# Kernel optimization log

Hardware: AMD Instinct MI355X
Metric: run time of the kernel (lower is better)

The kernel has to match this reference:

```python
import jax, jax.numpy as jnp
import numpy as np

DT_SCALER = 1.0 / 24.0
ODE_STEPS = 4  # fixed-step RK4 stand-in for adaptive odeint(rtol=atol=1e-3)
B, T, D, H = 1024, 100, 32, 256
ODE_MID = 50  # hidden width of the ODE func MLP (hard-coded 50 in source)


def setup_inputs() -> dict:
    key = jax.random.key(0)
    ks = jax.random.split(key, 20)
    n = lambda k, s: jax.random.normal(k, s, dtype=jnp.float32)
    std = 0.1  # module inits weights N(0, 0.1), biases 0
    return {
        "dt": jax.random.uniform(ks[0], (B, T, 2), dtype=jnp.float32),
        "x": n(ks[1], (B, T, D)),
        # RNNCell params
        "W_ih": n(ks[2], (H, D)) * std,
        "b_ih": jnp.zeros((H,), jnp.float32),
        "W_hh": n(ks[3], (H, H)) * std,
        "b_hh": jnp.zeros((H,), jnp.float32),
        # ODE func: Linear(H,50) -> tanh -> Linear(50,H)
        "ode_w1": n(ks[4], (ODE_MID, H)) * std,
        "ode_b1": jnp.zeros((ODE_MID,), jnp.float32),
        "ode_w2": n(ks[5], (H, ODE_MID)) * std,
        "ode_b2": jnp.zeros((H,), jnp.float32),
        # mu head: l1 (H -> H//2), distribution_mu (H//2 -> 1)
        "l1_w": n(ks[6], (H // 2, H)) * std,
        "l1_b": jnp.zeros((H // 2,), jnp.float32),
        "mu_w": n(ks[7], (1, H // 2)) * std,
        "mu_b": jnp.zeros((1,), jnp.float32),
        # sigma head: Linear(H,H) -> tanh -> Linear(H,1) -> softplus
        "sig_w1": n(ks[8], (H, H)) * std,
        "sig_b1": jnp.zeros((H,), jnp.float32),
        "sig_w2": n(ks[9], (1, H)) * std,
        "sig_b2": jnp.zeros((1,), jnp.float32),
    }


def reference(dt, x, W_ih, b_ih, W_hh, b_hh, ode_w1, ode_b1, ode_w2, ode_b2,
              l1_w, l1_b, mu_w, mu_b, sig_w1, sig_b1, sig_w2, sig_b2):
    Bsz = x.shape[0]
    xs = jnp.swapaxes(x, 0, 1)                               # [T,B,D]
    dts = jnp.swapaxes(dt[:, :, 1] - dt[:, :, 0], 0, 1)[..., None]  # [T,B,1]
    h0 = jnp.zeros((Bsz, W_hh.shape[0]), x.dtype)
    hs = 1.0 / ODE_STEPS

    def ode_f(y, scale):
        # net(y) * (dt * DT_SCALER); RHS is time-independent
        return (jnp.tanh(y @ ode_w1.T + ode_b1) @ ode_w2.T + ode_b2) * scale

    def step(h, inp):
        x_i, dt_i = inp                                      # [B,D], [B,1]
        # h_t = h_t + RNNCell(x_i, h_t)
        h = h + jnp.tanh(x_i @ W_ih.T + b_ih + h @ W_hh.T + b_hh)
        scale = dt_i * DT_SCALER
        # integrate dh/dt = ode_f(h) from t=0 to t=1 (fixed-step RK4)
        def rk4(y, _):
            k1 = ode_f(y, scale)
            k2 = ode_f(y + 0.5 * hs * k1, scale)
            k3 = ode_f(y + 0.5 * hs * k2, scale)
            k4 = ode_f(y + hs * k3, scale)
            return y + (hs / 6.0) * (k1 + 2.0 * k2 + 2.0 * k3 + k4), None
        h, _ = jax.lax.scan(rk4, h, None, length=ODE_STEPS)
        # heads (eval mode: dropout is identity)
        mu = jax.nn.relu(h @ l1_w.T + l1_b) @ mu_w.T + mu_b              # [B,1]
        sig = jax.nn.softplus(jnp.tanh(h @ sig_w1.T + sig_b1) @ sig_w2.T + sig_b2)
        return h, (mu, sig)

    _, (mu_seq, sig_seq) = jax.lax.scan(step, h0, (xs, dts))
    mu_out = jnp.swapaxes(mu_seq, 0, 1)    # [B,T,1]
    sig_out = jnp.swapaxes(sig_seq, 0, 1)  # [B,T,1]
    return (mu_out, sig_out)
```

## Files before the change

kernel.cpp:

```cpp
#include <hip/hip_runtime.h>
#include <math.h>


#define NT 512

#define WS_WCAT 0
#define WS_L1P  73728
#define WS_SW1  106496
#define WS_TOT  172032

#define F4_PR1P 0
#define F4_PR1Q 1088
#define F4_PR2P 2176
#define F4_PR2Q 3216
#define F4_PRR  2176
#define F4_PH1  0
#define F4_PH2  2176
#define F4_YCP  4256
#define F4_YCQ  4384
#define F4_MIDP 4512
#define F4_MIDQ 4544
#define F4_HS   4576
#define F4_XS   4832
#define F4_L1O  4864
#define F4_SG   4992
#define F4_END  5248
#define SM_BC   (F4_END * 4)
#define SM_OB1  (SM_BC + 256)
#define SM_OB2  (SM_OB1 + 64)
#define SM_L1B  (SM_OB2 + 256)
#define SM_SB1  (SM_L1B + 128)
#define SM_MUW  (SM_SB1 + 256)
#define SM_SW2  (SM_MUW + 128)
#define SM_SCL  (SM_SW2 + 256)
#define SM_TOTF (SM_SCL + 8)
#define SMEM_BYTES (SM_TOTF * 4)

__device__ __forceinline__ float fma4(float acc, float4 y, float4 w) {
  acc = fmaf(y.x, w.x, acc); acc = fmaf(y.y, w.y, acc);
  acc = fmaf(y.z, w.z, acc); acc = fmaf(y.w, w.w, acc);
  return acc;
}
__device__ __forceinline__ float4 add4(float4 a, float4 b) {
  return make_float4(a.x + b.x, a.y + b.y, a.z + b.z, a.w + b.w);
}
__device__ __forceinline__ float4 axpy4(float a, float4 xv, float4 yv) {
  return make_float4(fmaf(a, xv.x, yv.x), fmaf(a, xv.y, yv.y),
                     fmaf(a, xv.z, yv.z), fmaf(a, xv.w, yv.w));
}
__device__ __forceinline__ float4 muls4(float4 v, float s) {
  return make_float4(v.x * s, v.y * s, v.z * s, v.w * s);
}
__device__ __forceinline__ float tfast(float x) {
  float ax = fabsf(x);
  float e  = __expf(-2.f * ax);
  float t  = (1.f - e) * __builtin_amdgcn_rcpf(1.f + e);
  return copysignf(t, x);
}
__device__ __forceinline__ float4 tfast4(float4 v) {
  return make_float4(tfast(v.x), tfast(v.y), tfast(v.z), tfast(v.w));
}
template <int CTRL>
__device__ __forceinline__ float dpp_add(float v) {
  int s = __builtin_amdgcn_update_dpp(0, __float_as_int(v), CTRL, 0xF, 0xF, true);
  return v + __int_as_float(s);
}
__device__ __forceinline__ float4 red4f4(float4 v) {
  v.x = dpp_add<0xB1>(v.x); v.y = dpp_add<0xB1>(v.y);
  v.z = dpp_add<0xB1>(v.z); v.w = dpp_add<0xB1>(v.w);
  v.x = dpp_add<0x4E>(v.x); v.y = dpp_add<0x4E>(v.y);
  v.z = dpp_add<0x4E>(v.z); v.w = dpp_add<0x4E>(v.w);
  return v;
}

__global__ void prep_w(const float* __restrict__ Wih, const float* __restrict__ Whh,
                       const float* __restrict__ l1w, const float* __restrict__ sw1,
                       float* __restrict__ ws) {
  int i = blockIdx.x * 256 + threadIdx.x;
  if (i < 73728) {
    int g = i >> 10, rem = i & 1023, j = rem >> 2, c = rem & 3;
    int k = 4 * g + c;
    ws[i] = (k < 32) ? Wih[j * 32 + k] : Whh[j * 256 + (k - 32)];
  } else if (i < 106496) {
    int t = i - 73728;
    int g = t >> 9, rem = t & 511, j = rem >> 2, c = rem & 3;
    ws[i] = l1w[j * 256 + 4 * g + c];
  } else if (i < WS_TOT) {
    int t = i - 106496;
    int g = t >> 10, rem = t & 1023, j = rem >> 2, c = rem & 3;
    ws[i] = sw1[j * 256 + 4 * g + c];
  }
}

__global__ __attribute__((amdgpu_flat_work_group_size(NT, NT)))
void odernn_main(const float* __restrict__ dt,
                 const float* __restrict__ x,
                 const float* __restrict__ bih,
                 const float* __restrict__ bhh,
                 const float* __restrict__ ow1,
                 const float* __restrict__ ob1g,
                 const float* __restrict__ ow2,
                 const float* __restrict__ ob2g,
                 const float* __restrict__ l1bg,
                 const float* __restrict__ muwg,
                 const float* __restrict__ mubg,
                 const float* __restrict__ sb1g,
                 const float* __restrict__ sw2g,
                 const float* __restrict__ sb2g,
                 const float* __restrict__ ws,
                 float* __restrict__ out) {
  extern __shared__ __align__(16) float sm[];
  float4* f4 = (float4*)sm;
  const int tid = threadIdx.x;
  const int b0 = blockIdx.x * 4;

  const float4* wcat4 = (const float4*)(ws + WS_WCAT);
  const float4* l1w4  = (const float4*)(ws + WS_L1P);
  const float4* sw14  = (const float4*)(ws + WS_SW1);
  const float4* xg4   = (const float4*)x;

  const int q1 = tid & 15, kc1 = tid >> 4;
  const int cq2 = tid & 63, kc2 = tid >> 6;
  float4 w1r[4][2];
  float4 w2r[4][2];
  {
#pragma unroll
    for (int n = 0; n < 4; ++n) {
      int row = 4 * q1 + n;
#pragma unroll
      for (int g = 0; g < 2; ++g) {
        if (row < 50)
          w1r[n][g] = *(const float4*)&ow1[row * 256 + kc1 * 8 + 4 * g];
        else
          w1r[n][g] = make_float4(0.f, 0.f, 0.f, 0.f);
      }
    }
    float w2tmp[4];
#pragma unroll
    for (int n = 0; n < 4; ++n) {
      int col = 4 * cq2 + n;
#pragma unroll
      for (int g = 0; g < 2; ++g) {
#pragma unroll
        for (int c = 0; c < 4; ++c) {
          int k = kc2 * 8 + 4 * g + c;
          w2tmp[c] = (k < 50) ? ow2[col * 50 + k] : 0.f;
        }
        w2r[n][g] = make_float4(w2tmp[0], w2tmp[1], w2tmp[2], w2tmp[3]);
      }
    }
  }

  if (tid < 256) {
    sm[SM_BC + tid]  = bih[tid] + bhh[tid];
    sm[SM_OB2 + tid] = ob2g[tid];
    sm[SM_SB1 + tid] = sb1g[tid];
    sm[SM_SW2 + tid] = sw2g[tid];
  }
  if (tid < 64)  sm[SM_OB1 + tid] = (tid < 50) ? ob1g[tid] : 0.f;
  if (tid < 128) { sm[SM_L1B + tid] = l1bg[tid]; sm[SM_MUW + tid] = muwg[tid]; }
  if (tid < 256) f4[F4_HS + tid] = make_float4(0.f, 0.f, 0.f, 0.f);
  if (tid < 32) {
    int r = tid >> 3, g = tid & 7;
    f4[F4_XS + tid] = xg4[((size_t)(b0 + r) * 100) * 8 + g];
  } else if (tid < 36) {
    int r = tid - 32;
    const float* dp = dt + ((size_t)(b0 + r) * 100) * 2;
    sm[SM_SCL + r] = (dp[1] - dp[0]) * (1.f / 24.f);
  }
  __syncthreads();

  const float mubv = mubg[0], sb2v = sb2g[0];
  const float4* bc4   = (const float4*)(sm + SM_BC);
  const float4* ob1_4 = (const float4*)(sm + SM_OB1);
  const float4* ob2_4 = (const float4*)(sm + SM_OB2);
  const float4* l1b4  = (const float4*)(sm + SM_L1B);
  const float4* sb14  = (const float4*)(sm + SM_SB1);
  const float4* muw4  = (const float4*)(sm + SM_MUW);
  const float4* sw24  = (const float4*)(sm + SM_SW2);

  const int cqS = tid & 63, rxS = (tid >> 6) & 1;
  float4 hP = make_float4(0, 0, 0, 0), acP = hP, hQ = hP, acQ = hP;
  float scP = 0.f, scQ = 0.f;

  const int wv = tid >> 6, ln = tid & 63;

  auto L1PART = [&](int ycB, int prB) {
    float4 p0 = make_float4(0, 0, 0, 0), p1 = p0;
#pragma unroll
    for (int g = 0; g < 2; ++g) {
      float4 y0 = f4[ycB + kc1 * 2 + g];
      float4 y1 = f4[ycB + 64 + kc1 * 2 + g];
      p0.x = fma4(p0.x, y0, w1r[0][g]); p0.y = fma4(p0.y, y0, w1r[1][g]);
      p0.z = fma4(p0.z, y0, w1r[2][g]); p0.w = fma4(p0.w, y0, w1r[3][g]);
      p1.x = fma4(p1.x, y1, w1r[0][g]); p1.y = fma4(p1.y, y1, w1r[1][g]);
      p1.z = fma4(p1.z, y1, w1r[2][g]); p1.w = fma4(p1.w, y1, w1r[3][g]);
    }
    f4[prB + (kc1 * 2 + 0) * 17 + q1] = p0;
    f4[prB + (kc1 * 2 + 1) * 17 + q1] = p1;
  };
  auto L1RED = [&](int prB, int midB) {
    const int qr = (tid >> 2) & 15, sub = tid & 3, rx = tid >> 6;
    float4 v = make_float4(0, 0, 0, 0);
#pragma unroll
    for (int i = 0; i < 8; ++i)
      v = add4(v, f4[prB + ((sub * 8 + i) * 2 + rx) * 17 + qr]);
    v = red4f4(v);
    if (sub == 0)
      f4[midB + rx * 16 + qr] = tfast4(add4(v, ob1_4[qr]));
  };
  auto L2PART = [&](int midB, int prB) {
    float4 p0 = make_float4(0, 0, 0, 0), p1 = p0;
#pragma unroll
    for (int g = 0; g < 2; ++g) {
      float4 m0 = f4[midB + kc2 * 2 + g];
      float4 m1 = f4[midB + 16 + kc2 * 2 + g];
      p0.x = fma4(p0.x, m0, w2r[0][g]); p0.y = fma4(p0.y, m0, w2r[1][g]);
      p0.z = fma4(p0.z, m0, w2r[2][g]); p0.w = fma4(p0.w, m0, w2r[3][g]);
      p1.x = fma4(p1.x, m1, w2r[0][g]); p1.y = fma4(p1.y, m1, w2r[1][g]);
      p1.z = fma4(p1.z, m1, w2r[2][g]); p1.w = fma4(p1.w, m1, w2r[3][g]);
    }
    f4[prB + (kc2 * 2 + 0) * 65 + cq2] = p0;
    f4[prB + (kc2 * 2 + 1) * 65 + cq2] = p1;
  };
  auto L2RED = [&](float4& h, float4& ac, float sc, int prB, int ycB,
                   int hsRow, int e) {
    float4 v = ob2_4[cqS];
#pragma unroll
    for (int i = 0; i < 8; ++i)
      v = add4(v, f4[prB + (i * 2 + rxS) * 65 + cqS]);
    float4 kv = muls4(v, sc);
    const int s = e & 3;
    float4 ycw;
    if (s == 0) {
      ac = kv;                      ycw = axpy4(0.125f, kv, h);
    } else if (s == 1) {
      ac = axpy4(2.f, kv, ac);      ycw = axpy4(0.125f, kv, h);
    } else if (s == 2) {
      ac = axpy4(2.f, kv, ac);      ycw = axpy4(0.25f, kv, h);
    } else {
      h = axpy4(0.25f / 6.f, add4(ac, kv), h);
      ycw = h;
    }
    f4[ycB + rxS * 64 + cqS] = ycw;
    if (e == 15) f4[F4_HS + hsRow * 64 + cqS] = h;
  };

  for (int t = 0; t < 100; ++t) {
    {
      const int jq = tid & 63, kc = tid >> 6;
      float4 a0 = make_float4(0, 0, 0, 0), a1 = a0, a2 = a0, a3 = a0;
#pragma unroll 3
      for (int gg = 0; gg < 9; ++gg) {
        int g = kc * 9 + gg;
        float4 w0 = wcat4[g * 256 + 4 * jq + 0];
        float4 w1 = wcat4[g * 256 + 4 * jq + 1];
        float4 w2 = wcat4[g * 256 + 4 * jq + 2];
        float4 w3 = wcat4[g * 256 + 4 * jq + 3];
        float4 y0 = (g < 8) ? f4[F4_XS + g]      : f4[F4_HS + (g - 8)];
        float4 y1 = (g < 8) ? f4[F4_XS + 8 + g]  : f4[F4_HS + 64 + (g - 8)];
        float4 y2 = (g < 8) ? f4[F4_XS + 16 + g] : f4[F4_HS + 128 + (g - 8)];
        float4 y3 = (g < 8) ? f4[F4_XS + 24 + g] : f4[F4_HS + 192 + (g - 8)];
        a0.x = fma4(a0.x, y0, w0); a0.y = fma4(a0.y, y0, w1);
        a0.z = fma4(a0.z, y0, w2); a0.w = fma4(a0.w, y0, w3);
        a1.x = fma4(a1.x, y1, w0); a1.y = fma4(a1.y, y1, w1);
        a1.z = fma4(a1.z, y1, w2); a1.w = fma4(a1.w, y1, w3);
        a2.x = fma4(a2.x, y2, w0); a2.y = fma4(a2.y, y2, w1);
        a2.z = fma4(a2.z, y2, w2); a2.w = fma4(a2.w, y2, w3);
        a3.x = fma4(a3.x, y3, w0); a3.y = fma4(a3.y, y3, w1);
        a3.z = fma4(a3.z, y3, w2); a3.w = fma4(a3.w, y3, w3);
      }
      f4[F4_PRR + (kc * 4 + 0) * 65 + jq] = a0;
      f4[F4_PRR + (kc * 4 + 1) * 65 + jq] = a1;
      f4[F4_PRR + (kc * 4 + 2) * 65 + jq] = a2;
      f4[F4_PRR + (kc * 4 + 3) * 65 + jq] = a3;
    }
    __syncthreads();
    if (tid < 256) {
      const int r = tid >> 6, jq = tid & 63;
      float4 v = bc4[jq];
#pragma unroll
      for (int kc = 0; kc < 8; ++kc)
        v = add4(v, f4[F4_PRR + (kc * 4 + r) * 65 + jq]);
      float4 hn = add4(f4[F4_HS + r * 64 + jq], tfast4(v));
      if (r < 2) f4[F4_YCP + r * 64 + jq] = hn;
      else       f4[F4_YCQ + (r - 2) * 64 + jq] = hn;
    }
    __syncthreads();

#pragma unroll 1
    for (int e = 0; e < 16; ++e) {
      L1PART(F4_YCP, F4_PR1P);
      if (tid < 128) {
        if (e == 0) {
          hP = f4[F4_YCP + rxS * 64 + cqS];
          hQ = f4[F4_YCQ + rxS * 64 + cqS];
          acP = make_float4(0, 0, 0, 0); acQ = acP;
          scP = sm[SM_SCL + rxS];
          scQ = sm[SM_SCL + 2 + rxS];
        } else {
          L2RED(hQ, acQ, scQ, F4_PR2Q, F4_YCQ, 2 + rxS, e - 1);
        }
      }
      __syncthreads();
      L1PART(F4_YCQ, F4_PR1Q);
      if (tid < 128) L1RED(F4_PR1P, F4_MIDP);
      __syncthreads();
      L2PART(F4_MIDP, F4_PR2P);
      if (tid < 128) L1RED(F4_PR1Q, F4_MIDQ);
      __syncthreads();
      L2PART(F4_MIDQ, F4_PR2Q);
      if (tid < 128) L2RED(hP, acP, scP, F4_PR2P, F4_YCP, 0 + rxS, e);
      __syncthreads();
    }
    if (tid < 128) {
      L2RED(hQ, acQ, scQ, F4_PR2Q, F4_YCQ, 2 + rxS, 15);
    } else if (t < 99) {
      if (tid < 160) {
        int idx = tid - 128, r = idx >> 3, g = idx & 7;
        f4[F4_XS + idx] = xg4[((size_t)(b0 + r) * 100 + t + 1) * 8 + g];
      } else if (tid < 164) {
        int r = tid - 160;
        const float* dp = dt + ((size_t)(b0 + r) * 100 + t + 1) * 2;
        sm[SM_SCL + r] = (dp[1] - dp[0]) * (1.f / 24.f);
      }
    }
    __syncthreads();

    {
      const int cq = tid & 31, kc = tid >> 5;
      float4 c0 = make_float4(0, 0, 0, 0), c1 = c0, c2 = c0, c3 = c0;
#pragma unroll 2
      for (int g = 0; g < 4; ++g) {
        int kg = kc * 4 + g;
        float4 w0 = l1w4[kg * 128 + 4 * cq + 0];
        float4 w1 = l1w4[kg * 128 + 4 * cq + 1];
        float4 w2 = l1w4[kg * 128 + 4 * cq + 2];
        float4 w3 = l1w4[kg * 128 + 4 * cq + 3];
        float4 y0 = f4[F4_HS + kg],       y1 = f4[F4_HS + 64 + kg];
        float4 y2 = f4[F4_HS + 128 + kg], y3 = f4[F4_HS + 192 + kg];
        c0.x = fma4(c0.x, y0, w0); c0.y = fma4(c0.y, y0, w1);
        c0.z = fma4(c0.z, y0, w2); c0.w = fma4(c0.w, y0, w3);
        c1.x = fma4(c1.x, y1, w0); c1.y = fma4(c1.y, y1, w1);
        c1.z = fma4(c1.z, y1, w2); c1.w = fma4(c1.w, y1, w3);
        c2.x = fma4(c2.x, y2, w0); c2.y = fma4(c2.y, y2, w1);
        c2.z = fma4(c2.z, y2, w2); c2.w = fma4(c2.w, y2, w3);
        c3.x = fma4(c3.x, y3, w0); c3.y = fma4(c3.y, y3, w1);
        c3.z = fma4(c3.z, y3, w2); c3.w = fma4(c3.w, y3, w3);
      }
      f4[F4_PH1 + (kc * 4 + 0) * 33 + cq] = c0;
      f4[F4_PH1 + (kc * 4 + 1) * 33 + cq] = c1;
      f4[F4_PH1 + (kc * 4 + 2) * 33 + cq] = c2;
      f4[F4_PH1 + (kc * 4 + 3) * 33 + cq] = c3;
    }
    {
      const int cq = tid & 63, kc = tid >> 6;
      float4 d0 = make_float4(0, 0, 0, 0), d1 = d0, d2 = d0, d3 = d0;
#pragma unroll 2
      for (int g = 0; g < 8; ++g) {
        int kg = kc * 8 + g;
        float4 w0 = sw14[kg * 256 + 4 * cq + 0];
        float4 w1 = sw14[kg * 256 + 4 * cq + 1];
        float4 w2 = sw14[kg * 256 + 4 * cq + 2];
        float4 w3 = sw14[kg * 256 + 4 * cq + 3];
        float4 y0 = f4[F4_HS + kg],       y1 = f4[F4_HS + 64 + kg];
        float4 y2 = f4[F4_HS + 128 + kg], y3 = f4[F4_HS + 192 + kg];
        d0.x = fma4(d0.x, y0, w0); d0.y = fma4(d0.y, y0, w1);
        d0.z = fma4(d0.z, y0, w2); d0.w = fma4(d0.w, y0, w3);
        d1.x = fma4(d1.x, y1, w0); d1.y = fma4(d1.y, y1, w1);
        d1.z = fma4(d1.z, y1, w2); d1.w = fma4(d1.w, y1, w3);
        d2.x = fma4(d2.x, y2, w0); d2.y = fma4(d2.y, y2, w1);
        d2.z = fma4(d2.z, y2, w2); d2.w = fma4(d2.w, y2, w3);
        d3.x = fma4(d3.x, y3, w0); d3.y = fma4(d3.y, y3, w1);
        d3.z = fma4(d3.z, y3, w2); d3.w = fma4(d3.w, y3, w3);
      }
      f4[F4_PH2 + (kc * 4 + 0) * 65 + cq] = d0;
      f4[F4_PH2 + (kc * 4 + 1) * 65 + cq] = d1;
      f4[F4_PH2 + (kc * 4 + 2) * 65 + cq] = d2;
      f4[F4_PH2 + (kc * 4 + 3) * 65 + cq] = d3;
    }
    __syncthreads();
    if (tid < 128) {
      const int r = tid >> 5, cq = tid & 31;
      float4 v = l1b4[cq];
#pragma unroll
      for (int kc = 0; kc < 16; ++kc)
        v = add4(v, f4[F4_PH1 + (kc * 4 + r) * 33 + cq]);
      f4[F4_L1O + r * 32 + cq] =
          make_float4(fmaxf(v.x, 0.f), fmaxf(v.y, 0.f),
                      fmaxf(v.z, 0.f), fmaxf(v.w, 0.f));
    } else if (tid < 384) {
      const int t2 = tid - 128;
      const int r = t2 >> 6, cq = t2 & 63;
      float4 v = sb14[cq];
#pragma unroll
      for (int kc = 0; kc < 8; ++kc)
        v = add4(v, f4[F4_PH2 + (kc * 4 + r) * 65 + cq]);
      f4[F4_SG + r * 64 + cq] = tfast4(v);
    }
    __syncthreads();
    if (wv < 4) {
      float pm = 0.f;
      if (ln < 32) {
        float4 l = f4[F4_L1O + wv * 32 + ln];
        float4 w = muw4[ln];
        pm = l.x * w.x + l.y * w.y + l.z * w.z + l.w * w.w;
      }
#pragma unroll
      for (int off = 32; off > 0; off >>= 1) pm += __shfl_down(pm, off);
      if (ln == 0) out[(size_t)(b0 + wv) * 100 + t] = pm + mubv;
    } else {
      const int r = wv - 4;
      float4 sv = f4[F4_SG + r * 64 + ln];
      float4 w = sw24[ln];
      float ps = sv.x * w.x + sv.y * w.y + sv.z * w.z + sv.w * w.w;
#pragma unroll
      for (int off = 32; off > 0; off >>= 1) ps += __shfl_down(ps, off);
      if (ln == 0) {
        float z = ps + sb2v;
        float sp = fmaxf(z, 0.f) + log1pf(expf(-fabsf(z)));
        out[(size_t)102400 + (size_t)(b0 + r) * 100 + t] = sp;
      }
    }
    __syncthreads();
  }
}

extern "C" void kernel_launch(void* const* d_in, const int* in_sizes, int n_in,
                              void* d_out, int out_size, void* d_ws, size_t ws_size,
                              hipStream_t stream) {
  const float* dt  = (const float*)d_in[0];
  const float* x   = (const float*)d_in[1];
  const float* Wih = (const float*)d_in[2];
  const float* bih = (const float*)d_in[3];
  const float* Whh = (const float*)d_in[4];
  const float* bhh = (const float*)d_in[5];
  const float* ow1 = (const float*)d_in[6];
  const float* ob1 = (const float*)d_in[7];
  const float* ow2 = (const float*)d_in[8];
  const float* ob2 = (const float*)d_in[9];
  const float* l1w = (const float*)d_in[10];
  const float* l1b = (const float*)d_in[11];
  const float* muw = (const float*)d_in[12];
  const float* mub = (const float*)d_in[13];
  const float* sw1 = (const float*)d_in[14];
  const float* sb1 = (const float*)d_in[15];
  const float* sw2 = (const float*)d_in[16];
  const float* sb2 = (const float*)d_in[17];
  float* ws  = (float*)d_ws;
  float* out = (float*)d_out;

  hipFuncSetAttribute((const void*)odernn_main,
                      hipFuncAttributeMaxDynamicSharedMemorySize, SMEM_BYTES);

  prep_w<<<WS_TOT / 256, 256, 0, stream>>>(Wih, Whh, l1w, sw1, ws);
  odernn_main<<<256, NT, SMEM_BYTES, stream>>>(dt, x, bih, bhh, ow1, ob1, ow2, ob2,
                                               l1b, muw, mub, sb1, sw2, sb2, ws, out);
}
```

Measured before the change: 4.077 ms.

## Split ODE MLP layers across wave pairs with register-resident weights

Halves the block to 256 threads. Even waves now compute the first ODE layer (H→50, tanh) for one batch row while odd waves compute the second layer and the RK4 update for the other row, so the two layers run as a ping-pong pipeline over 33 phases per time step. Both ODE weight matrices are staged once in shared memory and reloaded into registers each step, and the layer-1 partial sums are reduced across lanes with DPP instead of through shared memory. This removes shared-memory partial-sum round trips and some barriers, at the cost of heavy register pressure (52 float4 weights per thread) and half as many threads for the RNN and head matmuls.

After: 3.323 ms. -18.5%, faster.

```diff
diff --git a/kernel.cpp b/kernel.cpp
--- a/kernel.cpp
+++ b/kernel.cpp
@@ -2,54 +2,48 @@
 #include <math.h>
 
 
-#define NT 512
+#define NT 256
 
 #define WS_WCAT 0
 #define WS_L1P  73728
 #define WS_SW1  106496
 #define WS_TOT  172032
 
-#define F4_PR1P 0
-#define F4_PR1Q 1088
-#define F4_PR2P 2176
-#define F4_PR2Q 3216
-#define F4_PRR  2176
-#define F4_PH1  0
-#define F4_PH2  2176
-#define F4_YCP  4256
-#define F4_YCQ  4384
-#define F4_MIDP 4512
-#define F4_MIDQ 4544
-#define F4_HS   4576
-#define F4_XS   4832
-#define F4_L1O  4864
-#define F4_SG   4992
-#define F4_END  5248
-#define SM_BC   (F4_END * 4)
-#define SM_OB1  (SM_BC + 256)
-#define SM_OB2  (SM_OB1 + 64)
-#define SM_L1B  (SM_OB2 + 256)
-#define SM_SB1  (SM_L1B + 128)
-#define SM_MUW  (SM_SB1 + 256)
-#define SM_SW2  (SM_MUW + 128)
-#define SM_SCL  (SM_SW2 + 256)
-#define SM_TOTF (SM_SCL + 8)
-#define SMEM_BYTES (SM_TOTF * 4)
-
-__device__ __forceinline__ float fma4(float acc, float4 y, float4 w) {
-  acc = fmaf(y.x, w.x, acc); acc = fmaf(y.y, w.y, acc);
-  acc = fmaf(y.z, w.z, acc); acc = fmaf(y.w, w.w, acc);
-  return acc;
+#define F4_YC   0
+#define F4_MID  256
+#define F4_PRR  320
+#define F4_PH1  320
+#define F4_PH2  1376
+#define F4_XS   2416
+#define F4_L1O  2448
+#define F4_SG   2576
+#define F4_W1   2832
+#define F4_W2   6160
+#define F4_END  9488
+#define SM_BC   (F4_END*4)
+#define SM_OB2  (SM_BC+256)
+#define SM_L1B  (SM_OB2+256)
+#define SM_SB1  (SM_L1B+128)
+#define SM_MUW  (SM_SB1+256)
+#define SM_SW2  (SM_MUW+128)
+#define SM_SCL  (SM_SW2+256)
+#define SM_TOTF (SM_SCL+4)
+#define SMEM_BYTES (SM_TOTF*4)
+
+__device__ __forceinline__ float fma4(float a, float4 y, float4 w) {
+  a = fmaf(y.x, w.x, a); a = fmaf(y.y, w.y, a);
+  a = fmaf(y.z, w.z, a); a = fmaf(y.w, w.w, a);
+  return a;
 }
 __device__ __forceinline__ float4 add4(float4 a, float4 b) {
-  return make_float4(a.x + b.x, a.y + b.y, a.z + b.z, a.w + b.w);
+  return make_float4(a.x+b.x, a.y+b.y, a.z+b.z, a.w+b.w);
 }
 __device__ __forceinline__ float4 axpy4(float a, float4 xv, float4 yv) {
-  return make_float4(fmaf(a, xv.x, yv.x), fmaf(a, xv.y, yv.y),
-                     fmaf(a, xv.z, yv.z), fmaf(a, xv.w, yv.w));
+  return make_float4(fmaf(a,xv.x,yv.x), fmaf(a,xv.y,yv.y),
+                     fmaf(a,xv.z,yv.z), fmaf(a,xv.w,yv.w));
 }
 __device__ __forceinline__ float4 muls4(float4 v, float s) {
-  return make_float4(v.x * s, v.y * s, v.z * s, v.w * s);
+  return make_float4(v.x*s, v.y*s, v.z*s, v.w*s);
 }
 __device__ __forceinline__ float tfast(float x) {
   float ax = fabsf(x);
@@ -65,12 +59,8 @@
   int s = __builtin_amdgcn_update_dpp(0, __float_as_int(v), CTRL, 0xF, 0xF, true);
   return v + __int_as_float(s);
 }
-__device__ __forceinline__ float4 red4f4(float4 v) {
-  v.x = dpp_add<0xB1>(v.x); v.y = dpp_add<0xB1>(v.y);
-  v.z = dpp_add<0xB1>(v.z); v.w = dpp_add<0xB1>(v.w);
-  v.x = dpp_add<0x4E>(v.x); v.y = dpp_add<0x4E>(v.y);
-  v.z = dpp_add<0x4E>(v.z); v.w = dpp_add<0x4E>(v.w);
-  return v;
+__device__ __forceinline__ float red16(float v) {
+  return dpp_add<0xB1>(dpp_add<0x4E>(dpp_add<0x141>(dpp_add<0x140>(v))));
 }
 
 __global__ void prep_w(const float* __restrict__ Wih, const float* __restrict__ Whh,
@@ -111,55 +101,40 @@
                  float* __restrict__ out) {
   extern __shared__ __align__(16) float sm[];
   float4* f4 = (float4*)sm;
+  float* midS = sm + F4_MID * 4;
   const int tid = threadIdx.x;
+  const int wv = tid >> 6, ln = tid & 63;
   const int b0 = blockIdx.x * 4;
+  const bool isA = (wv & 1) == 0;
+  const int ra = (wv >> 1) * 2, rb = ra + 1;
 
   const float4* wcat4 = (const float4*)(ws + WS_WCAT);
   const float4* l1w4  = (const float4*)(ws + WS_L1P);
   const float4* sw14  = (const float4*)(ws + WS_SW1);
   const float4* xg4   = (const float4*)x;
 
-  const int q1 = tid & 15, kc1 = tid >> 4;
-  const int cq2 = tid & 63, kc2 = tid >> 6;
-  float4 w1r[4][2];
-  float4 w2r[4][2];
-  {
-#pragma unroll
-    for (int n = 0; n < 4; ++n) {
-      int row = 4 * q1 + n;
-#pragma unroll
-      for (int g = 0; g < 2; ++g) {
-        if (row < 50)
-          w1r[n][g] = *(const float4*)&ow1[row * 256 + kc1 * 8 + 4 * g];
-        else
-          w1r[n][g] = make_float4(0.f, 0.f, 0.f, 0.f);
-      }
-    }
-    float w2tmp[4];
-#pragma unroll
-    for (int n = 0; n < 4; ++n) {
-      int col = 4 * cq2 + n;
-#pragma unroll
-      for (int g = 0; g < 2; ++g) {
-#pragma unroll
-        for (int c = 0; c < 4; ++c) {
-          int k = kc2 * 8 + 4 * g + c;
-          w2tmp[c] = (k < 50) ? ow2[col * 50 + k] : 0.f;
-        }
-        w2r[n][g] = make_float4(w2tmp[0], w2tmp[1], w2tmp[2], w2tmp[3]);
-      }
-    }
+  for (int i = tid; i < 3328; i += NT) {
+    int j = i >> 6, rem = i & 63, f = rem >> 4, kq = rem & 15;
+    float4 v = make_float4(0.f, 0.f, 0.f, 0.f);
+    if (j < 50) v = *(const float4*)&ow1[j * 256 + kq * 16 + 4 * f];
+    f4[F4_W1 + (j * 4 + f) * 16 + kq] = v;
   }
-
-  if (tid < 256) {
-    sm[SM_BC + tid]  = bih[tid] + bhh[tid];
-    sm[SM_OB2 + tid] = ob2g[tid];
-    sm[SM_SB1 + tid] = sb1g[tid];
-    sm[SM_SW2 + tid] = sw2g[tid];
+  for (int i = tid; i < 3328; i += NT) {
+    int cg = i >> 6, lq = i & 63;
+    int C = cg / 13, g = cg - C * 13;
+    int col = 4 * lq + C;
+    float t0 = (4*g+0 < 50) ? ow2[col*50 + 4*g+0] : 0.f;
+    float t1 = (4*g+1 < 50) ? ow2[col*50 + 4*g+1] : 0.f;
+    float t2 = (4*g+2 < 50) ? ow2[col*50 + 4*g+2] : 0.f;
+    float t3 = (4*g+3 < 50) ? ow2[col*50 + 4*g+3] : 0.f;
+    f4[F4_W2 + i] = make_float4(t0, t1, t2, t3);
   }
-  if (tid < 64)  sm[SM_OB1 + tid] = (tid < 50) ? ob1g[tid] : 0.f;
+  sm[SM_BC + tid]  = bih[tid] + bhh[tid];
+  sm[SM_OB2 + tid] = ob2g[tid];
+  sm[SM_SB1 + tid] = sb1g[tid];
+  sm[SM_SW2 + tid] = sw2g[tid];
   if (tid < 128) { sm[SM_L1B + tid] = l1bg[tid]; sm[SM_MUW + tid] = muwg[tid]; }
-  if (tid < 256) f4[F4_HS + tid] = make_float4(0.f, 0.f, 0.f, 0.f);
+  f4[F4_YC + tid] = make_float4(0.f, 0.f, 0.f, 0.f);
   if (tid < 32) {
     int r = tid >> 3, g = tid & 7;
     f4[F4_XS + tid] = xg4[((size_t)(b0 + r) * 100) * 8 + g];
@@ -171,174 +146,62 @@
   __syncthreads();
 
   const float mubv = mubg[0], sb2v = sb2g[0];
-  const float4* bc4   = (const float4*)(sm + SM_BC);
-  const float4* ob1_4 = (const float4*)(sm + SM_OB1);
-  const float4* ob2_4 = (const float4*)(sm + SM_OB2);
-  const float4* l1b4  = (const float4*)(sm + SM_L1B);
-  const float4* sb14  = (const float4*)(sm + SM_SB1);
-  const float4* muw4  = (const float4*)(sm + SM_MUW);
-  const float4* sw24  = (const float4*)(sm + SM_SW2);
-
-  const int cqS = tid & 63, rxS = (tid >> 6) & 1;
-  float4 hP = make_float4(0, 0, 0, 0), acP = hP, hQ = hP, acQ = hP;
-  float scP = 0.f, scQ = 0.f;
-
-  const int wv = tid >> 6, ln = tid & 63;
-
-  auto L1PART = [&](int ycB, int prB) {
-    float4 p0 = make_float4(0, 0, 0, 0), p1 = p0;
-#pragma unroll
-    for (int g = 0; g < 2; ++g) {
-      float4 y0 = f4[ycB + kc1 * 2 + g];
-      float4 y1 = f4[ycB + 64 + kc1 * 2 + g];
-      p0.x = fma4(p0.x, y0, w1r[0][g]); p0.y = fma4(p0.y, y0, w1r[1][g]);
-      p0.z = fma4(p0.z, y0, w1r[2][g]); p0.w = fma4(p0.w, y0, w1r[3][g]);
-      p1.x = fma4(p1.x, y1, w1r[0][g]); p1.y = fma4(p1.y, y1, w1r[1][g]);
-      p1.z = fma4(p1.z, y1, w1r[2][g]); p1.w = fma4(p1.w, y1, w1r[3][g]);
-    }
-    f4[prB + (kc1 * 2 + 0) * 17 + q1] = p0;
-    f4[prB + (kc1 * 2 + 1) * 17 + q1] = p1;
+  const float4* bc4  = (const float4*)(sm + SM_BC);
+  const float4* l1b4 = (const float4*)(sm + SM_L1B);
+  const float4* sb14 = (const float4*)(sm + SM_SB1);
+  const float4* muw4 = (const float4*)(sm + SM_MUW);
+  const float4* sw24 = (const float4*)(sm + SM_SW2);
+
+  auto RNNPART = [&]() {
+    const int jq = tid & 63, kc = tid >> 6;
+    float4 a0 = make_float4(0,0,0,0), a1 = a0, a2 = a0, a3 = a0;
+#pragma unroll 2
+    for (int gg = 0; gg < 18; ++gg) {
+      int g = kc * 18 + gg;
+      float4 w0 = wcat4[g * 256 + 4 * jq + 0];
+      float4 w1 = wcat4[g * 256 + 4 * jq + 1];
+      float4 w2 = wcat4[g * 256 + 4 * jq + 2];
+      float4 w3 = wcat4[g * 256 + 4 * jq + 3];
+      float4 y0 = (g < 8) ? f4[F4_XS + g]      : f4[F4_YC + (g - 8)];
+      float4 y1 = (g < 8) ? f4[F4_XS + 8 + g]  : f4[F4_YC + 64 + (g - 8)];
+      float4 y2 = (g < 8) ? f4[F4_XS + 16 + g] : f4[F4_YC + 128 + (g - 8)];
+      float4 y3 = (g < 8) ? f4[F4_XS + 24 + g] : f4[F4_YC + 192 + (g - 8)];
+      a0.x = fma4(a0.x, y0, w0); a0.y = fma4(a0.y, y0, w1);
+      a0.z = fma4(a0.z, y0, w2); a0.w = fma4(a0.w, y0, w3);
+      a1.x = fma4(a1.x, y1, w0); a1.y = fma4(a1.y, y1, w1);
+      a1.z = fma4(a1.z, y1, w2); a1.w = fma4(a1.w, y1, w3);
+      a2.x = fma4(a2.x, y2, w0); a2.y = fma4(a2.y, y2, w1);
+      a2.z = fma4(a2.z, y2, w2); a2.w = fma4(a2.w, y2, w3);
+      a3.x = fma4(a3.x, y3, w0); a3.y = fma4(a3.y, y3, w1);
+      a3.z = fma4(a3.z, y3, w2); a3.w = fma4(a3.w, y3, w3);
+    }
+    f4[F4_PRR + (kc * 4 + 0) * 65 + jq] = a0;
+    f4[F4_PRR + (kc * 4 + 1) * 65 + jq] = a1;
+    f4[F4_PRR + (kc * 4 + 2) * 65 + jq] = a2;
+    f4[F4_PRR + (kc * 4 + 3) * 65 + jq] = a3;
   };
-  auto L1RED = [&](int prB, int midB) {
-    const int qr = (tid >> 2) & 15, sub = tid & 3, rx = tid >> 6;
-    float4 v = make_float4(0, 0, 0, 0);
-#pragma unroll
-    for (int i = 0; i < 8; ++i)
-      v = add4(v, f4[prB + ((sub * 8 + i) * 2 + rx) * 17 + qr]);
-    v = red4f4(v);
-    if (sub == 0)
-      f4[midB + rx * 16 + qr] = tfast4(add4(v, ob1_4[qr]));
+  auto RNNRED = [&]() {
+    const int r = tid >> 6, jq = tid & 63;
+    float4 v = bc4[jq];
+#pragma unroll
+    for (int kc = 0; kc < 4; ++kc)
+      v = add4(v, f4[F4_PRR + (kc * 4 + r) * 65 + jq]);
+    float4 hold = f4[F4_YC + r * 64 + jq];
+    f4[F4_YC + r * 64 + jq] = add4(hold, tfast4(v));
   };
-  auto L2PART = [&](int midB, int prB) {
-    float4 p0 = make_float4(0, 0, 0, 0), p1 = p0;
-#pragma unroll
-    for (int g = 0; g < 2; ++g) {
-      float4 m0 = f4[midB + kc2 * 2 + g];
-      float4 m1 = f4[midB + 16 + kc2 * 2 + g];
-      p0.x = fma4(p0.x, m0, w2r[0][g]); p0.y = fma4(p0.y, m0, w2r[1][g]);
-      p0.z = fma4(p0.z, m0, w2r[2][g]); p0.w = fma4(p0.w, m0, w2r[3][g]);
-      p1.x = fma4(p1.x, m1, w2r[0][g]); p1.y = fma4(p1.y, m1, w2r[1][g]);
-      p1.z = fma4(p1.z, m1, w2r[2][g]); p1.w = fma4(p1.w, m1, w2r[3][g]);
-    }
-    f4[prB + (kc2 * 2 + 0) * 65 + cq2] = p0;
-    f4[prB + (kc2 * 2 + 1) * 65 + cq2] = p1;
-  };
-  auto L2RED = [&](float4& h, float4& ac, float sc, int prB, int ycB,
-                   int hsRow, int e) {
-    float4 v = ob2_4[cqS];
-#pragma unroll
-    for (int i = 0; i < 8; ++i)
-      v = add4(v, f4[prB + (i * 2 + rxS) * 65 + cqS]);
-    float4 kv = muls4(v, sc);
-    const int s = e & 3;
-    float4 ycw;
-    if (s == 0) {
-      ac = kv;                      ycw = axpy4(0.125f, kv, h);
-    } else if (s == 1) {
-      ac = axpy4(2.f, kv, ac);      ycw = axpy4(0.125f, kv, h);
-    } else if (s == 2) {
-      ac = axpy4(2.f, kv, ac);      ycw = axpy4(0.25f, kv, h);
-    } else {
-      h = axpy4(0.25f / 6.f, add4(ac, kv), h);
-      ycw = h;
-    }
-    f4[ycB + rxS * 64 + cqS] = ycw;
-    if (e == 15) f4[F4_HS + hsRow * 64 + cqS] = h;
-  };
-
-  for (int t = 0; t < 100; ++t) {
-    {
-      const int jq = tid & 63, kc = tid >> 6;
-      float4 a0 = make_float4(0, 0, 0, 0), a1 = a0, a2 = a0, a3 = a0;
-#pragma unroll 3
-      for (int gg = 0; gg < 9; ++gg) {
-        int g = kc * 9 + gg;
-        float4 w0 = wcat4[g * 256 + 4 * jq + 0];
-        float4 w1 = wcat4[g * 256 + 4 * jq + 1];
-        float4 w2 = wcat4[g * 256 + 4 * jq + 2];
-        float4 w3 = wcat4[g * 256 + 4 * jq + 3];
-        float4 y0 = (g < 8) ? f4[F4_XS + g]      : f4[F4_HS + (g - 8)];
-        float4 y1 = (g < 8) ? f4[F4_XS + 8 + g]  : f4[F4_HS + 64 + (g - 8)];
-        float4 y2 = (g < 8) ? f4[F4_XS + 16 + g] : f4[F4_HS + 128 + (g - 8)];
-        float4 y3 = (g < 8) ? f4[F4_XS + 24 + g] : f4[F4_HS + 192 + (g - 8)];
-        a0.x = fma4(a0.x, y0, w0); a0.y = fma4(a0.y, y0, w1);
-        a0.z = fma4(a0.z, y0, w2); a0.w = fma4(a0.w, y0, w3);
-        a1.x = fma4(a1.x, y1, w0); a1.y = fma4(a1.y, y1, w1);
-        a1.z = fma4(a1.z, y1, w2); a1.w = fma4(a1.w, y1, w3);
-        a2.x = fma4(a2.x, y2, w0); a2.y = fma4(a2.y, y2, w1);
-        a2.z = fma4(a2.z, y2, w2); a2.w = fma4(a2.w, y2, w3);
-        a3.x = fma4(a3.x, y3, w0); a3.y = fma4(a3.y, y3, w1);
-        a3.z = fma4(a3.z, y3, w2); a3.w = fma4(a3.w, y3, w3);
-      }
-      f4[F4_PRR + (kc * 4 + 0) * 65 + jq] = a0;
-      f4[F4_PRR + (kc * 4 + 1) * 65 + jq] = a1;
-      f4[F4_PRR + (kc * 4 + 2) * 65 + jq] = a2;
-      f4[F4_PRR + (kc * 4 + 3) * 65 + jq] = a3;
-    }
-    __syncthreads();
-    if (tid < 256) {
-      const int r = tid >> 6, jq = tid & 63;
-      float4 v = bc4[jq];
-#pragma unroll
-      for (int kc = 0; kc < 8; ++kc)
-        v = add4(v, f4[F4_PRR + (kc * 4 + r) * 65 + jq]);
-      float4 hn = add4(f4[F4_HS + r * 64 + jq], tfast4(v));
-      if (r < 2) f4[F4_YCP + r * 64 + jq] = hn;
-      else       f4[F4_YCQ + (r - 2) * 64 + jq] = hn;
-    }
-    __syncthreads();
-
-#pragma unroll 1
-    for (int e = 0; e < 16; ++e) {
-      L1PART(F4_YCP, F4_PR1P);
-      if (tid < 128) {
-        if (e == 0) {
-          hP = f4[F4_YCP + rxS * 64 + cqS];
-          hQ = f4[F4_YCQ + rxS * 64 + cqS];
-          acP = make_float4(0, 0, 0, 0); acQ = acP;
-          scP = sm[SM_SCL + rxS];
-          scQ = sm[SM_SCL + 2 + rxS];
-        } else {
-          L2RED(hQ, acQ, scQ, F4_PR2Q, F4_YCQ, 2 + rxS, e - 1);
-        }
-      }
-      __syncthreads();
-      L1PART(F4_YCQ, F4_PR1Q);
-      if (tid < 128) L1RED(F4_PR1P, F4_MIDP);
-      __syncthreads();
-      L2PART(F4_MIDP, F4_PR2P);
-      if (tid < 128) L1RED(F4_PR1Q, F4_MIDQ);
-      __syncthreads();
-      L2PART(F4_MIDQ, F4_PR2Q);
-      if (tid < 128) L2RED(hP, acP, scP, F4_PR2P, F4_YCP, 0 + rxS, e);
-      __syncthreads();
-    }
-    if (tid < 128) {
-      L2RED(hQ, acQ, scQ, F4_PR2Q, F4_YCQ, 2 + rxS, 15);
-    } else if (t < 99) {
-      if (tid < 160) {
-        int idx = tid - 128, r = idx >> 3, g = idx & 7;
-        f4[F4_XS + idx] = xg4[((size_t)(b0 + r) * 100 + t + 1) * 8 + g];
-      } else if (tid < 164) {
-        int r = tid - 160;
-        const float* dp = dt + ((size_t)(b0 + r) * 100 + t + 1) * 2;
-        sm[SM_SCL + r] = (dp[1] - dp[0]) * (1.f / 24.f);
-      }
-    }
-    __syncthreads();
-
+  auto HEADSPART = [&]() {
     {
       const int cq = tid & 31, kc = tid >> 5;
-      float4 c0 = make_float4(0, 0, 0, 0), c1 = c0, c2 = c0, c3 = c0;
+      float4 c0 = make_float4(0,0,0,0), c1 = c0, c2 = c0, c3 = c0;
 #pragma unroll 2
-      for (int g = 0; g < 4; ++g) {
-        int kg = kc * 4 + g;
+      for (int g = 0; g < 8; ++g) {
+        int kg = kc * 8 + g;
         float4 w0 = l1w4[kg * 128 + 4 * cq + 0];
         float4 w1 = l1w4[kg * 128 + 4 * cq + 1];
         float4 w2 = l1w4[kg * 128 + 4 * cq + 2];
         float4 w3 = l1w4[kg * 128 + 4 * cq + 3];
-        float4 y0 = f4[F4_HS + kg],       y1 = f4[F4_HS + 64 + kg];
-        float4 y2 = f4[F4_HS + 128 + kg], y3 = f4[F4_HS + 192 + kg];
+        float4 y0 = f4[F4_YC + kg],       y1 = f4[F4_YC + 64 + kg];
+        float4 y2 = f4[F4_YC + 128 + kg], y3 = f4[F4_YC + 192 + kg];
         c0.x = fma4(c0.x, y0, w0); c0.y = fma4(c0.y, y0, w1);
         c0.z = fma4(c0.z, y0, w2); c0.w = fma4(c0.w, y0, w3);
         c1.x = fma4(c1.x, y1, w0); c1.y = fma4(c1.y, y1, w1);
@@ -355,16 +218,16 @@
     }
     {
       const int cq = tid & 63, kc = tid >> 6;
-      float4 d0 = make_float4(0, 0, 0, 0), d1 = d0, d2 = d0, d3 = d0;
+      float4 d0 = make_float4(0,0,0,0), d1 = d0, d2 = d0, d3 = d0;
 #pragma unroll 2
-      for (int g = 0; g < 8; ++g) {
-        int kg = kc * 8 + g;
+      for (int g = 0; g < 16; ++g) {
+        int kg = kc * 16 + g;
         float4 w0 = sw14[kg * 256 + 4 * cq + 0];
         float4 w1 = sw14[kg * 256 + 4 * cq + 1];
         float4 w2 = sw14[kg * 256 + 4 * cq + 2];
         float4 w3 = sw14[kg * 256 + 4 * cq + 3];
-        float4 y0 = f4[F4_HS + kg],       y1 = f4[F4_HS + 64 + kg];
-        float4 y2 = f4[F4_HS + 128 + kg], y3 = f4[F4_HS + 192 + kg];
+        float4 y0 = f4[F4_YC + kg],       y1 = f4[F4_YC + 64 + kg];
+        float4 y2 = f4[F4_YC + 128 + kg], y3 = f4[F4_YC + 192 + kg];
         d0.x = fma4(d0.x, y0, w0); d0.y = fma4(d0.y, y0, w1);
         d0.z = fma4(d0.z, y0, w2); d0.w = fma4(d0.w, y0, w3);
         d1.x = fma4(d1.x, y1, w0); d1.y = fma4(d1.y, y1, w1);
@@ -379,50 +242,167 @@
       f4[F4_PH2 + (kc * 4 + 2) * 65 + cq] = d2;
       f4[F4_PH2 + (kc * 4 + 3) * 65 + cq] = d3;
     }
-    __syncthreads();
+  };
+  auto HEADSRED = [&]() {
     if (tid < 128) {
-      const int r = tid >> 5, cq = tid & 31;
+      int r = tid >> 5, cq = tid & 31;
       float4 v = l1b4[cq];
 #pragma unroll
-      for (int kc = 0; kc < 16; ++kc)
+      for (int kc = 0; kc < 8; ++kc)
         v = add4(v, f4[F4_PH1 + (kc * 4 + r) * 33 + cq]);
       f4[F4_L1O + r * 32 + cq] =
           make_float4(fmaxf(v.x, 0.f), fmaxf(v.y, 0.f),
                       fmaxf(v.z, 0.f), fmaxf(v.w, 0.f));
-    } else if (tid < 384) {
-      const int t2 = tid - 128;
-      const int r = t2 >> 6, cq = t2 & 63;
+    }
+    {
+      int r = tid >> 6, cq = tid & 63;
       float4 v = sb14[cq];
 #pragma unroll
-      for (int kc = 0; kc < 8; ++kc)
+      for (int kc = 0; kc < 4; ++kc)
         v = add4(v, f4[F4_PH2 + (kc * 4 + r) * 65 + cq]);
       f4[F4_SG + r * 64 + cq] = tfast4(v);
     }
-    __syncthreads();
-    if (wv < 4) {
-      float pm = 0.f;
-      if (ln < 32) {
-        float4 l = f4[F4_L1O + wv * 32 + ln];
-        float4 w = muw4[ln];
-        pm = l.x * w.x + l.y * w.y + l.z * w.z + l.w * w.w;
-      }
-#pragma unroll
-      for (int off = 32; off > 0; off >>= 1) pm += __shfl_down(pm, off);
-      if (ln == 0) out[(size_t)(b0 + wv) * 100 + t] = pm + mubv;
-    } else {
-      const int r = wv - 4;
-      float4 sv = f4[F4_SG + r * 64 + ln];
-      float4 w = sw24[ln];
-      float ps = sv.x * w.x + sv.y * w.y + sv.z * w.z + sv.w * w.w;
-#pragma unroll
-      for (int off = 32; off > 0; off >>= 1) ps += __shfl_down(ps, off);
-      if (ln == 0) {
-        float z = ps + sb2v;
-        float sp = fmaxf(z, 0.f) + log1pf(expf(-fabsf(z)));
-        out[(size_t)102400 + (size_t)(b0 + r) * 100 + t] = sp;
-      }
-    }
-    __syncthreads();
+  };
+  auto DOTS = [&](int t) {
+    float pm = 0.f;
+    if (ln < 32) {
+      float4 l = f4[F4_L1O + wv * 32 + ln];
+      float4 w = muw4[ln];
+      pm = l.x * w.x + l.y * w.y + l.z * w.z + l.w * w.w;
+    }
+#pragma unroll
+    for (int off = 32; off > 0; off >>= 1) pm += __shfl_down(pm, off);
+    if (ln == 0) out[(size_t)(b0 + wv) * 100 + t] = pm + mubv;
+    float4 sv = f4[F4_SG + wv * 64 + ln];
+    float4 w2v = sw24[ln];
+    float ps = sv.x * w2v.x + sv.y * w2v.y + sv.z * w2v.z + sv.w * w2v.w;
+#pragma unroll
+    for (int off = 32; off > 0; off >>= 1) ps += __shfl_down(ps, off);
+    if (ln == 0) {
+      float z = ps + sb2v;
+      float sp = fmaxf(z, 0.f) + log1pf(expf(-fabsf(z)));
+      out[(size_t)102400 + (size_t)(b0 + wv) * 100 + t] = sp;
+    }
+  };
+
+  if (isA) {
+    const int qA = ln >> 4, kcA = ln & 15;
+    float4 w1r[13][4];
+    float ob1A = 0.f;
+    {
+      int jb = qA * 13 + kcA;
+      if (kcA < 13 && jb < 50) ob1A = ob1g[jb];
+    }
+    auto L1 = [&](int row) {
+      const float4* ycr = f4 + F4_YC + row * 64 + kcA * 4;
+      float4 y0 = ycr[0], y1 = ycr[1], y2 = ycr[2], y3 = ycr[3];
+      float p[13];
+#pragma unroll
+      for (int jj = 0; jj < 13; ++jj) {
+        float s = 0.f;
+        s = fma4(s, y0, w1r[jj][0]); s = fma4(s, y1, w1r[jj][1]);
+        s = fma4(s, y2, w1r[jj][2]); s = fma4(s, y3, w1r[jj][3]);
+        p[jj] = s;
+      }
+#pragma unroll
+      for (int jj = 0; jj < 13; ++jj) p[jj] = red16(p[jj]);
+      if (kcA < 13) {
+        float v = p[0];
+#pragma unroll
+        for (int jj = 1; jj < 13; ++jj) v = (kcA == jj) ? p[jj] : v;
+        midS[row * 64 + qA * 13 + kcA] = tfast(v + ob1A);
+      }
+    };
+
+    for (int t = 0; t < 100; ++t) {
+      RNNPART();  __syncthreads();
+      RNNRED();   __syncthreads();
+#pragma unroll
+      for (int jj = 0; jj < 13; ++jj)
+#pragma unroll
+        for (int f = 0; f < 4; ++f)
+          w1r[jj][f] = f4[F4_W1 + ((qA * 13 + jj) * 4 + f) * 16 + kcA];
+#pragma unroll 1
+      for (int ph = 0; ph <= 32; ++ph) {
+        if (ph < 32) {
+          L1(ra + (ph & 1));
+        } else if (t < 99 && wv == 0) {
+          if (ln < 32) {
+            int r = ln >> 3, g = ln & 7;
+            f4[F4_XS + ln] = xg4[((size_t)(b0 + r) * 100 + t + 1) * 8 + g];
+          } else if (ln < 36) {
+            int r = ln - 32;
+            const float* dp = dt + ((size_t)(b0 + r) * 100 + t + 1) * 2;
+            sm[SM_SCL + r] = (dp[1] - dp[0]) * (1.f / 24.f);
+          }
+        }
+        __syncthreads();
+      }
+      HEADSPART(); __syncthreads();
+      HEADSRED();  __syncthreads();
+      DOTS(t);     __syncthreads();
+    }
+  } else {
+    float4 w2c0[13], w2c1[13], w2c2[13], w2c3[13];
+    float4 hA, hB, acA, acB;
+    float sclA = 0.f, sclB = 0.f;
+    auto L2 = [&](int row, int e, float4& h, float4& ac, float sc) {
+      const float4* mr = (const float4*)(midS + row * 64);
+      float bx = 0.f, by = 0.f, bz = 0.f, bw = 0.f;
+#define L2STEP(mv, g) bx = fma4(bx, mv, w2c0[g]); by = fma4(by, mv, w2c1[g]); \
+                      bz = fma4(bz, mv, w2c2[g]); bw = fma4(bw, mv, w2c3[g]);
+      {
+        float4 a0 = mr[0], a1 = mr[1], a2 = mr[2], a3 = mr[3], a4 = mr[4];
+        L2STEP(a0, 0) L2STEP(a1, 1) L2STEP(a2, 2) L2STEP(a3, 3) L2STEP(a4, 4)
+      }
+      {
+        float4 a0 = mr[5], a1 = mr[6], a2 = mr[7], a3 = mr[8];
+        L2STEP(a0, 5) L2STEP(a1, 6) L2STEP(a2, 7) L2STEP(a3, 8)
+      }
+      {
+        float4 a0 = mr[9], a1 = mr[10], a2 = mr[11], a3 = mr[12];
+        L2STEP(a0, 9) L2STEP(a1, 10) L2STEP(a2, 11) L2STEP(a3, 12)
+      }
+#undef L2STEP
+      float4 ob2v = ((const float4*)(sm + SM_OB2))[ln];
+      float4 kv = muls4(add4(make_float4(bx, by, bz, bw), ob2v), sc);
+      const int s = e & 3;
+      float4 ycw;
+      if (s == 0)      { ac = kv;                 ycw = axpy4(0.125f, kv, h); }
+      else if (s == 1) { ac = axpy4(2.f, kv, ac); ycw = axpy4(0.125f, kv, h); }
+      else if (s == 2) { ac = axpy4(2.f, kv, ac); ycw = axpy4(0.25f,  kv, h); }
+      else             { h = axpy4(0.25f / 6.f, add4(ac, kv), h); ycw = h; }
+      f4[F4_YC + row * 64 + ln] = ycw;
+    };
+
+    for (int t = 0; t < 100; ++t) {
+      RNNPART();  __syncthreads();
+      RNNRED();   __syncthreads();
+#pragma unroll
+      for (int g = 0; g < 13; ++g) {
+        w2c0[g] = f4[F4_W2 + (0 * 13 + g) * 64 + ln];
+        w2c1[g] = f4[F4_W2 + (1 * 13 + g) * 64 + ln];
+        w2c2[g] = f4[F4_W2 + (2 * 13 + g) * 64 + ln];
+        w2c3[g] = f4[F4_W2 + (3 * 13 + g) * 64 + ln];
+      }
+#pragma unroll 1
+      for (int ph = 0; ph <= 32; ++ph) {
+        if (ph == 0) {
+          hA = f4[F4_YC + ra * 64 + ln];
+          hB = f4[F4_YC + rb * 64 + ln];
+          acA = make_float4(0.f, 0.f, 0.f, 0.f); acB = acA;
+          sclA = sm[SM_SCL + ra]; sclB = sm[SM_SCL + rb];
+        } else if (ph & 1) {
+          L2(ra, (ph - 1) >> 1, hA, acA, sclA);
+        } else {
+          L2(rb, (ph - 2) >> 1, hB, acB, sclB);
+        }
+        __syncthreads();
+      }
+      HEADSPART(); __syncthreads();
+      HEADSRED();  __syncthreads();
+      DOTS(t);     __syncthreads();
+    }
   }
 }
 
```
